# Optimization experiments

Hardware: AMD Instinct MI355X
Metric: run time of the kernel (lower is better)

The kernel has to match this reference:

```python
import jax, jax.numpy as jnp
import numpy as np

N_NODES = 50000


def _sage_conv(x, src, dst, Wl, Wr, b):
    """SAGEConv with mean aggregation: lin_l(mean_j x_j) + lin_r(x_i) + b."""
    msgs = x[src]                                                # [E, Din] gather
    agg = jax.ops.segment_sum(msgs, dst, num_segments=N_NODES)  # [N, Din] scatter-add
    cnt = jax.ops.segment_sum(jnp.ones((src.shape[0], 1), x.dtype), dst,
                              num_segments=N_NODES)             # [N, 1]
    agg = agg / jnp.maximum(cnt, 1.0)                           # mean
    return agg @ Wl.T + x @ Wr.T + b                            # [N, Dout]


def setup_inputs() -> dict:
    key = jax.random.key(0)
    ks = jax.random.split(key, 8)
    d_in, d_h = 64, 128
    x = jax.random.normal(ks[0], (N_NODES, d_in), dtype=jnp.float32)
    edge_index = jax.random.randint(ks[1], (2, 800000), 0, N_NODES, dtype=jnp.int32)
    s1 = 1.0 / np.sqrt(d_in)
    s2 = 1.0 / np.sqrt(d_h)
    return {
        "x": x,
        "edge_index": edge_index,
        "Wl1": jax.random.normal(ks[2], (d_h, d_in), dtype=jnp.float32) * s1,
        "Wr1": jax.random.normal(ks[3], (d_h, d_in), dtype=jnp.float32) * s1,
        "b1": jnp.zeros((d_h,), dtype=jnp.float32),
        "Wl2": jax.random.normal(ks[4], (d_h, d_h), dtype=jnp.float32) * s2,
        "Wr2": jax.random.normal(ks[5], (d_h, d_h), dtype=jnp.float32) * s2,
        "b2": jnp.zeros((d_h,), dtype=jnp.float32),
    }


def reference(x, edge_index, Wl1, Wr1, b1, Wl2, Wr2, b2):
    src, dst = edge_index[0], edge_index[1]
    # layer 1: conv -> dropout(eval: identity) -> ReLU
    h = jax.nn.relu(_sage_conv(x, src, dst, Wl1, Wr1, b1))
    # layer 2
    h = jax.nn.relu(_sage_conv(h, src, dst, Wl2, Wr2, b2))
    return h
```

## Files before the change

kernel.cpp:

```cpp
#include <hip/hip_runtime.h>

#define N_NODES 50000
#define NBUCK 391
#define BCAP 4096
#define BSHIFT 12

typedef __attribute__((ext_vector_type(8))) short short8;
typedef __attribute__((ext_vector_type(4))) float floatx4;

static __device__ __forceinline__ unsigned short f2bf(float f) {
  unsigned int u = __builtin_bit_cast(unsigned int, f);
  u += 0x7fff + ((u >> 16) & 1);
  return (unsigned short)(u >> 16);
}
static __device__ __forceinline__ float bf2f(unsigned short s) {
  unsigned int u = ((unsigned int)s) << 16;
  return __builtin_bit_cast(float, u);
}


__global__ void __launch_bounds__(1024) prep_scatter(
    const float* __restrict__ x,
    const float* __restrict__ Wl1, const float* __restrict__ Wr1,
    const float* __restrict__ Wl2, const float* __restrict__ Wr2,
    unsigned short* __restrict__ A1, unsigned short* __restrict__ W1,
    unsigned short* __restrict__ W2,
    const int* __restrict__ src, const int* __restrict__ dst,
    int* __restrict__ bucket_cur, int* __restrict__ buf, int E, int n) {
  const int t = threadIdx.x;
  const int gid = blockIdx.x * 1024 + t;
  const int gsz = gridDim.x * 1024;
  for (int i = gid; i < n * 64; i += gsz)
    A1[(size_t)(i >> 6) * 128 + 64 + (i & 63)] = f2bf(x[i]);
  for (int i = gid; i < 128 * 128; i += gsz) {
    int c = i >> 7, k = i & 127;
    W1[i] = f2bf(k < 64 ? Wl1[c * 64 + k] : Wr1[c * 64 + k - 64]);
  }
  for (int i = gid; i < 128 * 256; i += gsz) {
    int c = i >> 8, k = i & 255;
    W2[i] = f2bf(k < 128 ? Wl2[c * 128 + k] : Wr2[c * 128 + k - 128]);
  }

  __shared__ int hist[NBUCK];
  __shared__ int base_s[NBUCK];
  for (int i = t; i < NBUCK; i += 1024) hist[i] = 0;
  __syncthreads();
  int e0 = blockIdx.x * 4096;
  int sv[4], dv[4], bv[4];
#pragma unroll
  for (int p = 0; p < 4; ++p) {
    int e = e0 + p * 1024 + t;
    if (e < E) {
      sv[p] = src[e];
      dv[p] = dst[e];
      bv[p] = dv[p] >> 7;
      atomicAdd(&hist[bv[p]], 1);
    } else bv[p] = -1;
  }
  __syncthreads();
  for (int i = t; i < NBUCK; i += 1024) {
    int c = hist[i];
    base_s[i] = c > 0 ? atomicAdd(&bucket_cur[i], c) : 0;
  }
  __syncthreads();
  for (int i = t; i < NBUCK; i += 1024) hist[i] = 0;
  __syncthreads();
#pragma unroll
  for (int p = 0; p < 4; ++p) {
    if (bv[p] >= 0) {
      int sub = base_s[bv[p]] + atomicAdd(&hist[bv[p]], 1);
      if (sub < BCAP) buf[(bv[p] << BSHIFT) + sub] = (sv[p] << 7) | (dv[p] & 127);
    }
  }
}


__global__ void __launch_bounds__(1024) bucket_csr_agg64(
    int* __restrict__ buf, const int* __restrict__ bucket_cur,
    int* __restrict__ row_start, int* __restrict__ row_cnt,
    unsigned short* __restrict__ A1, int n) {
  __shared__ int eb[BCAP];
  __shared__ int cnt[128];
  __shared__ int tmp[128];
  __shared__ int cur[128];
  const int t = threadIdx.x;
  const int b = blockIdx.x;
  const int node0 = b << 7;
  const int len = min(bucket_cur[b], BCAP);
  int* reg = buf + (b << BSHIFT);
  if (t < 128) cnt[t] = 0;
  __syncthreads();
  for (int i = t; i < len; i += 1024) {
    int p = reg[i];
    eb[i] = p;
    atomicAdd(&cnt[p & 127], 1);
  }
  __syncthreads();
  if (t < 128) tmp[t] = cnt[t];
  __syncthreads();
#pragma unroll
  for (int off = 1; off < 128; off <<= 1) {
    int u = (t >= off && t < 128) ? tmp[t - off] : 0;
    __syncthreads();
    if (t < 128) tmp[t] += u;
    __syncthreads();
  }
  if (t < 128) {
    int ex = tmp[t] - cnt[t];
    cur[t] = ex;
    int nd = node0 + t;
    if (nd < n) {
      row_start[nd] = (b << BSHIFT) + ex;
      row_cnt[nd] = cnt[t];
    }
  }
  __syncthreads();
  for (int i = t; i < len; i += 1024) {
    int p = eb[i];
    int sub = atomicAdd(&cur[p & 127], 1);
    reg[sub] = p >> 7;
  }
  __syncthreads();
  const int lane = t & 63;
  const int wv = t >> 6;
  const int eq = lane >> 3;
  const int cl = lane & 7;
  for (int loc = wv; loc < 128; loc += 16) {
    int nd = node0 + loc;
    if (nd >= n) break;
    int cn = cnt[loc];
    const int* sp = reg + (tmp[loc] - cn);
    float acc[8];
#pragma unroll
    for (int j = 0; j < 8; ++j) acc[j] = 0.f;
    for (int e = 0; e < cn; e += 8) {
      if (e + eq < cn) {
        int s = sp[e + eq];
        short8 v = *(const short8*)(A1 + (size_t)s * 128 + 64 + cl * 8);
#pragma unroll
        for (int j = 0; j < 8; ++j) acc[j] += bf2f((unsigned short)v[j]);
      }
    }
#pragma unroll
    for (int j = 0; j < 8; ++j) {
      acc[j] += __shfl_xor(acc[j], 8, 64);
      acc[j] += __shfl_xor(acc[j], 16, 64);
      acc[j] += __shfl_xor(acc[j], 32, 64);
    }
    if (eq == 0) {
      float inv = 1.0f / (float)max(cn, 1);
      short8 o;
#pragma unroll
      for (int j = 0; j < 8; ++j) o[j] = (short)f2bf(acc[j] * inv);
      *(short8*)(A1 + (size_t)nd * 128 + cl * 8) = o;
    }
  }
}


__global__ void agg_mean128(unsigned short* __restrict__ A2,
    const int* __restrict__ row_start, const int* __restrict__ row_cnt,
    const int* __restrict__ srcs, int n) {
  int wid = (blockIdx.x * blockDim.x + threadIdx.x) >> 6;
  int lane = threadIdx.x & 63;
  if (wid >= n) return;
  int start = row_start[wid];
  int cnt = row_cnt[wid];
  const int eq = lane >> 4;
  const int cl = lane & 15;
  float acc[8];
#pragma unroll
  for (int j = 0; j < 8; ++j) acc[j] = 0.f;
  for (int e = 0; e < cnt; e += 4) {
    if (e + eq < cnt) {
      int s = srcs[start + e + eq];
      short8 v = *(const short8*)(A2 + (size_t)s * 256 + 128 + cl * 8);
#pragma unroll
      for (int j = 0; j < 8; ++j) acc[j] += bf2f((unsigned short)v[j]);
    }
  }
#pragma unroll
  for (int j = 0; j < 8; ++j) {
    acc[j] += __shfl_xor(acc[j], 16, 64);
    acc[j] += __shfl_xor(acc[j], 32, 64);
  }
  if (eq == 0) {
    float inv = 1.0f / (float)max(cnt, 1);
    short8 o;
#pragma unroll
    for (int j = 0; j < 8; ++j) o[j] = (short)f2bf(acc[j] * inv);
    *(short8*)(A2 + (size_t)wid * 256 + cl * 8) = o;
  }
}


template<int KP, bool BF_OUT>
__global__ void __launch_bounds__(256) mfma_gemm(
    const unsigned short* __restrict__ A, const unsigned short* __restrict__ W,
    const float* __restrict__ bias, unsigned short* __restrict__ outb,
    float* __restrict__ outf, int n, int ostride, int ocol) {
  const int lane = threadIdx.x & 63;
  const int wv = threadIdx.x >> 6;
  const int m = lane & 15;
  const int q = lane >> 4;
  const int r0 = blockIdx.x * 128 + wv * 32;

  floatx4 acc[2][8];
#pragma unroll
  for (int rt = 0; rt < 2; ++rt)
#pragma unroll
    for (int ct = 0; ct < 8; ++ct) acc[rt][ct] = (floatx4){0.f, 0.f, 0.f, 0.f};

  int ra = r0 + m;      if (ra > n - 1) ra = n - 1;
  int rb = r0 + 16 + m; if (rb > n - 1) rb = n - 1;
  const unsigned short* Arow0 = A + (size_t)ra * KP + q * 8;
  const unsigned short* Arow1 = A + (size_t)rb * KP + q * 8;
  const unsigned short* Wrow  = W + (size_t)m * KP + q * 8;

#pragma unroll 1
  for (int kc = 0; kc < KP / 32; ++kc) {
    short8 a0 = *(const short8*)(Arow0 + kc * 32);
    short8 a1 = *(const short8*)(Arow1 + kc * 32);
#pragma unroll
    for (int ct = 0; ct < 8; ++ct) {
      short8 wf = *(const short8*)(Wrow + (size_t)ct * 16 * KP + kc * 32);
      acc[0][ct] = __builtin_amdgcn_mfma_f32_16x16x32_bf16(a0, wf, acc[0][ct], 0, 0, 0);
      acc[1][ct] = __builtin_amdgcn_mfma_f32_16x16x32_bf16(a1, wf, acc[1][ct], 0, 0, 0);
    }
  }

  float bv[8];
#pragma unroll
  for (int ct = 0; ct < 8; ++ct) bv[ct] = bias[ct * 16 + m];

#pragma unroll
  for (int rt = 0; rt < 2; ++rt) {
#pragma unroll
    for (int j = 0; j < 4; ++j) {
      int row = r0 + rt * 16 + q * 4 + j;
      if (row < n) {
#pragma unroll
        for (int ct = 0; ct < 8; ++ct) {
          float v = acc[rt][ct][j] + bv[ct];
          v = v > 0.f ? v : 0.f;
          int col = ct * 16 + m;
          if (BF_OUT) outb[(size_t)row * ostride + ocol + col] = f2bf(v);
          else        outf[(size_t)row * ostride + col] = v;
        }
      }
    }
  }
}


extern "C" void kernel_launch(void* const* d_in, const int* in_sizes, int n_in,
                              void* d_out, int out_size, void* d_ws, size_t ws_size,
                              hipStream_t stream) {
  const int N = N_NODES;
  const int E = in_sizes[1] / 2;
  const float* x   = (const float*)d_in[0];
  const int*   src = (const int*)d_in[1];
  const int*   dst = src + E;
  const float* Wl1 = (const float*)d_in[2];
  const float* Wr1 = (const float*)d_in[3];
  const float* b1  = (const float*)d_in[4];
  const float* Wl2 = (const float*)d_in[5];
  const float* Wr2 = (const float*)d_in[6];
  const float* b2  = (const float*)d_in[7];
  float* out = (float*)d_out;

  unsigned short* A1 = (unsigned short*)d_ws;
  unsigned short* A2 = A1 + (size_t)N * 128;
  unsigned short* W1 = A2 + (size_t)N * 256;
  unsigned short* W2 = W1 + 128 * 128;
  int* row_start  = (int*)(W2 + 128 * 256);
  int* row_cnt    = row_start + N;
  int* bucket_cur = row_cnt + N;
  int* buf        = bucket_cur + 392;

  hipMemsetAsync(bucket_cur, 0, NBUCK * sizeof(int), stream);
  int sb = (E + 4095) / 4096;
  prep_scatter<<<sb, 1024, 0, stream>>>(x, Wl1, Wr1, Wl2, Wr2, A1, W1, W2,
                                        src, dst, bucket_cur, buf, E, N);
  bucket_csr_agg64<<<NBUCK, 1024, 0, stream>>>(buf, bucket_cur, row_start, row_cnt, A1, N);

  int gb = (N + 127) / 128;
  mfma_gemm<128, true><<<gb, 256, 0, stream>>>(A1, W1, b1, A2, nullptr, N, 256, 128);

  int ab = (N * 64 + 255) / 256;
  agg_mean128<<<ab, 256, 0, stream>>>(A2, row_start, row_cnt, buf, N);
  mfma_gemm<256, false><<<gb, 256, 0, stream>>>(A2, W2, b2, nullptr, out, N, 128, 0);
}
```

Before: 200.6 us.

## Fuse neighbor aggregation with MFMA GEMM per 128-node block via shared memory

Each layer's mean aggregation is merged with its linear transform into a single kernel. Aggregated rows are staged in LDS and fed straight into MFMA, while self features are read from compact bf16 buffers. This drops two launches and the global round trip of the aggregated activations, and the gather loops are unrolled two-way to keep more loads in flight. In exchange, GEMM2 now runs on only 391 blocks of 1024 threads with LDS-limited occupancy, and the compute phase waits behind the irregular gather.

Result: faster. 193.8 us (-3.4%).

```diff
diff --git a/kernel.cpp b/kernel.cpp
--- a/kernel.cpp
+++ b/kernel.cpp
@@ -23,15 +23,14 @@
     const float* __restrict__ x,
     const float* __restrict__ Wl1, const float* __restrict__ Wr1,
     const float* __restrict__ Wl2, const float* __restrict__ Wr2,
-    unsigned short* __restrict__ A1, unsigned short* __restrict__ W1,
+    unsigned short* __restrict__ xb, unsigned short* __restrict__ W1,
     unsigned short* __restrict__ W2,
     const int* __restrict__ src, const int* __restrict__ dst,
     int* __restrict__ bucket_cur, int* __restrict__ buf, int E, int n) {
   const int t = threadIdx.x;
   const int gid = blockIdx.x * 1024 + t;
   const int gsz = gridDim.x * 1024;
-  for (int i = gid; i < n * 64; i += gsz)
-    A1[(size_t)(i >> 6) * 128 + 64 + (i & 63)] = f2bf(x[i]);
+  for (int i = gid; i < n * 64; i += gsz) xb[i] = f2bf(x[i]);
   for (int i = gid; i < 128 * 128; i += gsz) {
     int c = i >> 7, k = i & 127;
     W1[i] = f2bf(k < 64 ? Wl1[c * 64 + k] : Wr1[c * 64 + k - 64]);
@@ -75,11 +74,13 @@
 }
 
 
-__global__ void __launch_bounds__(1024) bucket_csr_agg64(
+__global__ void __launch_bounds__(1024) csr_agg_gemm1(
     int* __restrict__ buf, const int* __restrict__ bucket_cur,
     int* __restrict__ row_start, int* __restrict__ row_cnt,
-    unsigned short* __restrict__ A1, int n) {
+    const unsigned short* __restrict__ xb, const unsigned short* __restrict__ W1,
+    const float* __restrict__ b1, unsigned short* __restrict__ h1, int n) {
   __shared__ int eb[BCAP];
+  __shared__ __align__(16) unsigned short aggS[128 * 72];
   __shared__ int cnt[128];
   __shared__ int tmp[128];
   __shared__ int cur[128];
@@ -88,6 +89,7 @@
   const int node0 = b << 7;
   const int len = min(bucket_cur[b], BCAP);
   int* reg = buf + (b << BSHIFT);
+
   if (t < 128) cnt[t] = 0;
   __syncthreads();
   for (int i = t; i < len; i += 1024) {
@@ -121,132 +123,217 @@
     reg[sub] = p >> 7;
   }
   __syncthreads();
+
   const int lane = t & 63;
   const int wv = t >> 6;
   const int eq = lane >> 3;
   const int cl = lane & 7;
   for (int loc = wv; loc < 128; loc += 16) {
     int nd = node0 + loc;
-    if (nd >= n) break;
-    int cn = cnt[loc];
-    const int* sp = reg + (tmp[loc] - cn);
-    float acc[8];
-#pragma unroll
-    for (int j = 0; j < 8; ++j) acc[j] = 0.f;
-    for (int e = 0; e < cn; e += 8) {
+    int cn = (nd < n) ? cnt[loc] : 0;
+    const int* sp = reg + (tmp[loc] - cnt[loc]);
+    float ac[8], ac2[8];
+#pragma unroll
+    for (int j = 0; j < 8; ++j) { ac[j] = 0.f; ac2[j] = 0.f; }
+    int e = 0;
+    for (; e + 16 <= cn; e += 16) {
+      int s0 = sp[e + eq];
+      int s1 = sp[e + 8 + eq];
+      short8 v0 = *(const short8*)(xb + (size_t)s0 * 64 + cl * 8);
+      short8 v1 = *(const short8*)(xb + (size_t)s1 * 64 + cl * 8);
+#pragma unroll
+      for (int j = 0; j < 8; ++j) { ac[j] += bf2f((unsigned short)v0[j]); ac2[j] += bf2f((unsigned short)v1[j]); }
+    }
+    for (; e < cn; e += 8) {
       if (e + eq < cn) {
         int s = sp[e + eq];
-        short8 v = *(const short8*)(A1 + (size_t)s * 128 + 64 + cl * 8);
-#pragma unroll
-        for (int j = 0; j < 8; ++j) acc[j] += bf2f((unsigned short)v[j]);
+        short8 v = *(const short8*)(xb + (size_t)s * 64 + cl * 8);
+#pragma unroll
+        for (int j = 0; j < 8; ++j) ac[j] += bf2f((unsigned short)v[j]);
       }
     }
 #pragma unroll
     for (int j = 0; j < 8; ++j) {
-      acc[j] += __shfl_xor(acc[j], 8, 64);
-      acc[j] += __shfl_xor(acc[j], 16, 64);
-      acc[j] += __shfl_xor(acc[j], 32, 64);
+      ac[j] += ac2[j];
+      ac[j] += __shfl_xor(ac[j], 8, 64);
+      ac[j] += __shfl_xor(ac[j], 16, 64);
+      ac[j] += __shfl_xor(ac[j], 32, 64);
     }
     if (eq == 0) {
       float inv = 1.0f / (float)max(cn, 1);
       short8 o;
 #pragma unroll
-      for (int j = 0; j < 8; ++j) o[j] = (short)f2bf(acc[j] * inv);
-      *(short8*)(A1 + (size_t)nd * 128 + cl * 8) = o;
-    }
-  }
-}
-
-
-__global__ void agg_mean128(unsigned short* __restrict__ A2,
-    const int* __restrict__ row_start, const int* __restrict__ row_cnt,
-    const int* __restrict__ srcs, int n) {
-  int wid = (blockIdx.x * blockDim.x + threadIdx.x) >> 6;
-  int lane = threadIdx.x & 63;
-  if (wid >= n) return;
-  int start = row_start[wid];
-  int cnt = row_cnt[wid];
+      for (int j = 0; j < 8; ++j) o[j] = (short)f2bf(ac[j] * inv);
+      *(short8*)(aggS + loc * 72 + cl * 8) = o;
+    }
+  }
+  __syncthreads();
+
+  const int m = lane & 15;
+  const int q = lane >> 4;
+  const int rw = (wv & 3) * 32;
+  const int cw = (wv >> 2) * 32;
+  floatx4 acc[2][2];
+#pragma unroll
+  for (int rt = 0; rt < 2; ++rt)
+#pragma unroll
+    for (int ct = 0; ct < 2; ++ct) acc[rt][ct] = (floatx4){0.f, 0.f, 0.f, 0.f};
+
+  int ra = node0 + rw + m;      if (ra > n - 1) ra = n - 1;
+  int rb = node0 + rw + 16 + m; if (rb > n - 1) rb = n - 1;
+  const unsigned short* selfA0 = xb + (size_t)ra * 64 + q * 8;
+  const unsigned short* selfA1 = xb + (size_t)rb * 64 + q * 8;
+  const unsigned short* aggL0 = aggS + (rw + m) * 72 + q * 8;
+  const unsigned short* aggL1 = aggS + (rw + 16 + m) * 72 + q * 8;
+  const unsigned short* Wc0 = W1 + (size_t)(cw + m) * 128 + q * 8;
+  const unsigned short* Wc1 = W1 + (size_t)(cw + 16 + m) * 128 + q * 8;
+
+#pragma unroll
+  for (int kc = 0; kc < 2; ++kc) {
+    short8 a0 = *(const short8*)(aggL0 + kc * 32);
+    short8 a1 = *(const short8*)(aggL1 + kc * 32);
+    short8 w0 = *(const short8*)(Wc0 + kc * 32);
+    short8 w1 = *(const short8*)(Wc1 + kc * 32);
+    acc[0][0] = __builtin_amdgcn_mfma_f32_16x16x32_bf16(a0, w0, acc[0][0], 0, 0, 0);
+    acc[0][1] = __builtin_amdgcn_mfma_f32_16x16x32_bf16(a0, w1, acc[0][1], 0, 0, 0);
+    acc[1][0] = __builtin_amdgcn_mfma_f32_16x16x32_bf16(a1, w0, acc[1][0], 0, 0, 0);
+    acc[1][1] = __builtin_amdgcn_mfma_f32_16x16x32_bf16(a1, w1, acc[1][1], 0, 0, 0);
+  }
+#pragma unroll
+  for (int kc = 0; kc < 2; ++kc) {
+    short8 a0 = *(const short8*)(selfA0 + kc * 32);
+    short8 a1 = *(const short8*)(selfA1 + kc * 32);
+    short8 w0 = *(const short8*)(Wc0 + 64 + kc * 32);
+    short8 w1 = *(const short8*)(Wc1 + 64 + kc * 32);
+    acc[0][0] = __builtin_amdgcn_mfma_f32_16x16x32_bf16(a0, w0, acc[0][0], 0, 0, 0);
+    acc[0][1] = __builtin_amdgcn_mfma_f32_16x16x32_bf16(a0, w1, acc[0][1], 0, 0, 0);
+    acc[1][0] = __builtin_amdgcn_mfma_f32_16x16x32_bf16(a1, w0, acc[1][0], 0, 0, 0);
+    acc[1][1] = __builtin_amdgcn_mfma_f32_16x16x32_bf16(a1, w1, acc[1][1], 0, 0, 0);
+  }
+
+  float bv0 = b1[cw + m], bv1 = b1[cw + 16 + m];
+#pragma unroll
+  for (int rt = 0; rt < 2; ++rt) {
+#pragma unroll
+    for (int j = 0; j < 4; ++j) {
+      int row = node0 + rw + rt * 16 + q * 4 + j;
+      if (row < n) {
+        float v0 = acc[rt][0][j] + bv0; v0 = v0 > 0.f ? v0 : 0.f;
+        float v1 = acc[rt][1][j] + bv1; v1 = v1 > 0.f ? v1 : 0.f;
+        h1[(size_t)row * 128 + cw + m] = f2bf(v0);
+        h1[(size_t)row * 128 + cw + 16 + m] = f2bf(v1);
+      }
+    }
+  }
+}
+
+
+__global__ void __launch_bounds__(1024) agg_gemm2(
+    const unsigned short* __restrict__ h1, const int* __restrict__ row_start,
+    const int* __restrict__ row_cnt, const int* __restrict__ buf,
+    const unsigned short* __restrict__ W2, const float* __restrict__ b2,
+    float* __restrict__ out, int n) {
+  __shared__ __align__(16) unsigned short aggS[128 * 136];
+  const int t = threadIdx.x;
+  const int lane = t & 63;
+  const int wv = t >> 6;
+  const int node0 = blockIdx.x << 7;
+
   const int eq = lane >> 4;
   const int cl = lane & 15;
-  float acc[8];
-#pragma unroll
-  for (int j = 0; j < 8; ++j) acc[j] = 0.f;
-  for (int e = 0; e < cnt; e += 4) {
-    if (e + eq < cnt) {
-      int s = srcs[start + e + eq];
-      short8 v = *(const short8*)(A2 + (size_t)s * 256 + 128 + cl * 8);
-#pragma unroll
-      for (int j = 0; j < 8; ++j) acc[j] += bf2f((unsigned short)v[j]);
-    }
-  }
-#pragma unroll
-  for (int j = 0; j < 8; ++j) {
-    acc[j] += __shfl_xor(acc[j], 16, 64);
-    acc[j] += __shfl_xor(acc[j], 32, 64);
-  }
-  if (eq == 0) {
-    float inv = 1.0f / (float)max(cnt, 1);
-    short8 o;
-#pragma unroll
-    for (int j = 0; j < 8; ++j) o[j] = (short)f2bf(acc[j] * inv);
-    *(short8*)(A2 + (size_t)wid * 256 + cl * 8) = o;
-  }
-}
-
-
-template<int KP, bool BF_OUT>
-__global__ void __launch_bounds__(256) mfma_gemm(
-    const unsigned short* __restrict__ A, const unsigned short* __restrict__ W,
-    const float* __restrict__ bias, unsigned short* __restrict__ outb,
-    float* __restrict__ outf, int n, int ostride, int ocol) {
-  const int lane = threadIdx.x & 63;
-  const int wv = threadIdx.x >> 6;
+  for (int loc = wv; loc < 128; loc += 16) {
+    int nd = node0 + loc;
+    int cn = 0, start = 0;
+    if (nd < n) { cn = row_cnt[nd]; start = row_start[nd]; }
+    float ac[8], ac2[8];
+#pragma unroll
+    for (int j = 0; j < 8; ++j) { ac[j] = 0.f; ac2[j] = 0.f; }
+    int e = 0;
+    for (; e + 8 <= cn; e += 8) {
+      int s0 = buf[start + e + eq];
+      int s1 = buf[start + e + 4 + eq];
+      short8 v0 = *(const short8*)(h1 + (size_t)s0 * 128 + cl * 8);
+      short8 v1 = *(const short8*)(h1 + (size_t)s1 * 128 + cl * 8);
+#pragma unroll
+      for (int j = 0; j < 8; ++j) { ac[j] += bf2f((unsigned short)v0[j]); ac2[j] += bf2f((unsigned short)v1[j]); }
+    }
+    for (; e < cn; e += 4) {
+      if (e + eq < cn) {
+        int s = buf[start + e + eq];
+        short8 v = *(const short8*)(h1 + (size_t)s * 128 + cl * 8);
+#pragma unroll
+        for (int j = 0; j < 8; ++j) ac[j] += bf2f((unsigned short)v[j]);
+      }
+    }
+#pragma unroll
+    for (int j = 0; j < 8; ++j) {
+      ac[j] += ac2[j];
+      ac[j] += __shfl_xor(ac[j], 16, 64);
+      ac[j] += __shfl_xor(ac[j], 32, 64);
+    }
+    if (eq == 0) {
+      float inv = 1.0f / (float)max(cn, 1);
+      short8 o;
+#pragma unroll
+      for (int j = 0; j < 8; ++j) o[j] = (short)f2bf(ac[j] * inv);
+      *(short8*)(aggS + loc * 136 + cl * 8) = o;
+    }
+  }
+  __syncthreads();
+
   const int m = lane & 15;
   const int q = lane >> 4;
-  const int r0 = blockIdx.x * 128 + wv * 32;
-
-  floatx4 acc[2][8];
+  const int rw = (wv & 3) * 32;
+  const int cw = (wv >> 2) * 32;
+  floatx4 acc[2][2];
 #pragma unroll
   for (int rt = 0; rt < 2; ++rt)
 #pragma unroll
-    for (int ct = 0; ct < 8; ++ct) acc[rt][ct] = (floatx4){0.f, 0.f, 0.f, 0.f};
-
-  int ra = r0 + m;      if (ra > n - 1) ra = n - 1;
-  int rb = r0 + 16 + m; if (rb > n - 1) rb = n - 1;
-  const unsigned short* Arow0 = A + (size_t)ra * KP + q * 8;
-  const unsigned short* Arow1 = A + (size_t)rb * KP + q * 8;
-  const unsigned short* Wrow  = W + (size_t)m * KP + q * 8;
-
-#pragma unroll 1
-  for (int kc = 0; kc < KP / 32; ++kc) {
-    short8 a0 = *(const short8*)(Arow0 + kc * 32);
-    short8 a1 = *(const short8*)(Arow1 + kc * 32);
-#pragma unroll
-    for (int ct = 0; ct < 8; ++ct) {
-      short8 wf = *(const short8*)(Wrow + (size_t)ct * 16 * KP + kc * 32);
-      acc[0][ct] = __builtin_amdgcn_mfma_f32_16x16x32_bf16(a0, wf, acc[0][ct], 0, 0, 0);
-      acc[1][ct] = __builtin_amdgcn_mfma_f32_16x16x32_bf16(a1, wf, acc[1][ct], 0, 0, 0);
-    }
-  }
-
-  float bv[8];
-#pragma unroll
-  for (int ct = 0; ct < 8; ++ct) bv[ct] = bias[ct * 16 + m];
-
+    for (int ct = 0; ct < 2; ++ct) acc[rt][ct] = (floatx4){0.f, 0.f, 0.f, 0.f};
+
+  int ra = node0 + rw + m;      if (ra > n - 1) ra = n - 1;
+  int rb = node0 + rw + 16 + m; if (rb > n - 1) rb = n - 1;
+  const unsigned short* selfA0 = h1 + (size_t)ra * 128 + q * 8;
+  const unsigned short* selfA1 = h1 + (size_t)rb * 128 + q * 8;
+  const unsigned short* aggL0 = aggS + (rw + m) * 136 + q * 8;
+  const unsigned short* aggL1 = aggS + (rw + 16 + m) * 136 + q * 8;
+  const unsigned short* Wc0 = W2 + (size_t)(cw + m) * 256 + q * 8;
+  const unsigned short* Wc1 = W2 + (size_t)(cw + 16 + m) * 256 + q * 8;
+
+#pragma unroll
+  for (int kc = 0; kc < 4; ++kc) {
+    short8 a0 = *(const short8*)(aggL0 + kc * 32);
+    short8 a1 = *(const short8*)(aggL1 + kc * 32);
+    short8 w0 = *(const short8*)(Wc0 + kc * 32);
+    short8 w1 = *(const short8*)(Wc1 + kc * 32);
+    acc[0][0] = __builtin_amdgcn_mfma_f32_16x16x32_bf16(a0, w0, acc[0][0], 0, 0, 0);
+    acc[0][1] = __builtin_amdgcn_mfma_f32_16x16x32_bf16(a0, w1, acc[0][1], 0, 0, 0);
+    acc[1][0] = __builtin_amdgcn_mfma_f32_16x16x32_bf16(a1, w0, acc[1][0], 0, 0, 0);
+    acc[1][1] = __builtin_amdgcn_mfma_f32_16x16x32_bf16(a1, w1, acc[1][1], 0, 0, 0);
+  }
+#pragma unroll
+  for (int kc = 0; kc < 4; ++kc) {
+    short8 a0 = *(const short8*)(selfA0 + kc * 32);
+    short8 a1 = *(const short8*)(selfA1 + kc * 32);
+    short8 w0 = *(const short8*)(Wc0 + 128 + kc * 32);
+    short8 w1 = *(const short8*)(Wc1 + 128 + kc * 32);
+    acc[0][0] = __builtin_amdgcn_mfma_f32_16x16x32_bf16(a0, w0, acc[0][0], 0, 0, 0);
+    acc[0][1] = __builtin_amdgcn_mfma_f32_16x16x32_bf16(a0, w1, acc[0][1], 0, 0, 0);
+    acc[1][0] = __builtin_amdgcn_mfma_f32_16x16x32_bf16(a1, w0, acc[1][0], 0, 0, 0);
+    acc[1][1] = __builtin_amdgcn_mfma_f32_16x16x32_bf16(a1, w1, acc[1][1], 0, 0, 0);
+  }
+
+  float bv0 = b2[cw + m], bv1 = b2[cw + 16 + m];
 #pragma unroll
   for (int rt = 0; rt < 2; ++rt) {
 #pragma unroll
     for (int j = 0; j < 4; ++j) {
-      int row = r0 + rt * 16 + q * 4 + j;
+      int row = node0 + rw + rt * 16 + q * 4 + j;
       if (row < n) {
-#pragma unroll
-        for (int ct = 0; ct < 8; ++ct) {
-          float v = acc[rt][ct][j] + bv[ct];
-          v = v > 0.f ? v : 0.f;
-          int col = ct * 16 + m;
-          if (BF_OUT) outb[(size_t)row * ostride + ocol + col] = f2bf(v);
-          else        outf[(size_t)row * ostride + col] = v;
-        }
+        float v0 = acc[rt][0][j] + bv0; v0 = v0 > 0.f ? v0 : 0.f;
+        float v1 = acc[rt][1][j] + bv1; v1 = v1 > 0.f ? v1 : 0.f;
+        out[(size_t)row * 128 + cw + m] = v0;
+        out[(size_t)row * 128 + cw + 16 + m] = v1;
       }
     }
   }
@@ -269,9 +356,9 @@
   const float* b2  = (const float*)d_in[7];
   float* out = (float*)d_out;
 
-  unsigned short* A1 = (unsigned short*)d_ws;
-  unsigned short* A2 = A1 + (size_t)N * 128;
-  unsigned short* W1 = A2 + (size_t)N * 256;
+  unsigned short* xb = (unsigned short*)d_ws;
+  unsigned short* h1 = xb + (size_t)N * 64;
+  unsigned short* W1 = h1 + (size_t)N * 128;
   unsigned short* W2 = W1 + 128 * 128;
   int* row_start  = (int*)(W2 + 128 * 256);
   int* row_cnt    = row_start + N;
@@ -280,14 +367,9 @@
 
   hipMemsetAsync(bucket_cur, 0, NBUCK * sizeof(int), stream);
   int sb = (E + 4095) / 4096;
-  prep_scatter<<<sb, 1024, 0, stream>>>(x, Wl1, Wr1, Wl2, Wr2, A1, W1, W2,
+  prep_scatter<<<sb, 1024, 0, stream>>>(x, Wl1, Wr1, Wl2, Wr2, xb, W1, W2,
                                         src, dst, bucket_cur, buf, E, N);
-  bucket_csr_agg64<<<NBUCK, 1024, 0, stream>>>(buf, bucket_cur, row_start, row_cnt, A1, N);
-
-  int gb = (N + 127) / 128;
-  mfma_gemm<128, true><<<gb, 256, 0, stream>>>(A1, W1, b1, A2, nullptr, N, 256, 128);
-
-  int ab = (N * 64 + 255) / 256;
-  agg_mean128<<<ab, 256, 0, stream>>>(A2, row_start, row_cnt, buf, N);
-  mfma_gemm<256, false><<<gb, 256, 0, stream>>>(A2, W2, b2, nullptr, out, N, 128, 0);
-}
+  csr_agg_gemm1<<<NBUCK, 1024, 0, stream>>>(buf, bucket_cur, row_start, row_cnt,
+                                            xb, W1, b1, h1, N);
+  agg_gemm2<<<NBUCK, 1024, 0, stream>>>(h1, row_start, row_cnt, buf, W2, b2, out, N);
+}
```
